# Kernel optimization log

Measured on AMD Instinct MI355X. Metric: run time of the kernel, lower is better.

Reference implementation:

```python
import jax, jax.numpy as jnp
import numpy as np

N, M = 50000, 2048          # nodes, observations
E, O = 512, 256             # in_features_embed, in_features_obs
EPS = 1e-6


def setup_inputs() -> dict:
    key = jax.random.key(0)
    k1, k2, k3, k4, k5 = jax.random.split(key, 5)
    scale_e = 1.0 / np.sqrt(E)
    scale_o = 1.0 / np.sqrt(O)
    return {
        "node_feature": jax.random.normal(k1, (N, E), dtype=jnp.float32),
        "obs_feature": jax.random.normal(k2, (M, O), dtype=jnp.float32),
        # nn.Linear weights, stored as [out, in] like torch
        "W_q": jax.random.normal(k3, (E, E), dtype=jnp.float32) * scale_e,
        "W_k": jax.random.normal(k4, (E, O), dtype=jnp.float32) * scale_o,
        "W_v": jax.random.normal(k5, (E, O), dtype=jnp.float32) * scale_o,
        "ln_gamma": jnp.ones((E,), dtype=jnp.float32),
        "ln_beta": jnp.zeros((E,), dtype=jnp.float32),
    }


def layer_norm(x, gamma, beta, eps=EPS):
    mu = jnp.mean(x, axis=-1, keepdims=True)
    var = jnp.mean(jnp.square(x - mu), axis=-1, keepdims=True)
    return (x - mu) * jax.lax.rsqrt(var + eps) * gamma + beta


def reference(node_feature, obs_feature, W_q, W_k, W_v, ln_gamma, ln_beta):
    # projections (torch Linear: x @ W.T)
    q = node_feature @ W_q.T            # [N, E]
    k = obs_feature @ W_k.T             # [M, E]
    v = obs_feature @ W_v.T             # [M, E]
    # un-normalized cross-attention (no softmax), original association
    attn = q @ k.T                      # [N, M]
    out = attn @ v                      # [N, E]
    return layer_norm(out + node_feature, ln_gamma, ln_beta)
```

## Files before the change

### kernel.cpp

```cpp
#include <hip/hip_runtime.h>
#include <hip/hip_bf16.h>

#define NROWS 50000
#define MOBS  2048
#define EDIM  512
#define ODIM  256

typedef short s16x8 __attribute__((ext_vector_type(8)));
typedef float f32x4 __attribute__((ext_vector_type(4)));

__device__ __forceinline__ unsigned short f32_to_bf16(float f) {
    unsigned int u = __float_as_uint(f);
    u += 0x7fffu + ((u >> 16) & 1u);
    return (unsigned short)(u >> 16);
}

template <int TA, int TB, int SPLIT, int FRAG>
__global__ __launch_bounds__(256) void sgemm4(const float* __restrict__ A,
                                              const float* __restrict__ B,
                                              void* __restrict__ Cv,
                                              int NN, int KK, int lda, int ldb) {
    __shared__ float SA[16][68];
    __shared__ float SB[16][68];
    const int t  = threadIdx.x;
    const int tx = t & 15, ty = t >> 4;
    const int i0 = blockIdx.y * 64, j0 = blockIdx.x * 64;
    int k_lo = 0, k_hi = KK;
    if (SPLIT > 1) { int ch = KK / SPLIT; k_lo = blockIdx.z * ch; k_hi = k_lo + ch; }

    float acc[4][4];
#pragma unroll
    for (int a = 0; a < 4; ++a)
#pragma unroll
        for (int b = 0; b < 4; ++b) acc[a][b] = 0.f;

    for (int k0 = k_lo; k0 < k_hi; k0 += 16) {
#pragma unroll
        for (int r = 0; r < 4; ++r) {
            int idx = t + 256 * r;
            int mm, kk2;
            if (TA) { mm = idx & 63; kk2 = idx >> 6; }
            else    { kk2 = idx & 15; mm = idx >> 4; }
            SA[kk2][mm] = TA ? A[(size_t)(k0 + kk2) * lda + i0 + mm]
                             : A[(size_t)(i0 + mm) * lda + k0 + kk2];
        }
#pragma unroll
        for (int r = 0; r < 4; ++r) {
            int idx = t + 256 * r;
            int jj, kk2;
            if (TB) { kk2 = idx & 15; jj = idx >> 4; }
            else    { jj = idx & 63; kk2 = idx >> 6; }
            SB[kk2][jj] = TB ? B[(size_t)(j0 + jj) * ldb + k0 + kk2]
                             : B[(size_t)(k0 + kk2) * ldb + j0 + jj];
        }
        __syncthreads();
#pragma unroll
        for (int kk2 = 0; kk2 < 16; ++kk2) {
            float4 a4 = *(const float4*)&SA[kk2][ty * 4];
            float4 b4 = *(const float4*)&SB[kk2][tx * 4];
            float av[4] = {a4.x, a4.y, a4.z, a4.w};
            float bv[4] = {b4.x, b4.y, b4.z, b4.w};
#pragma unroll
            for (int a = 0; a < 4; ++a)
#pragma unroll
                for (int b = 0; b < 4; ++b) acc[a][b] += av[a] * bv[b];
        }
        __syncthreads();
    }

    if (FRAG) {
        unsigned short* C = (unsigned short*)Cv;
#pragma unroll
        for (int a = 0; a < 4; ++a)
#pragma unroll
            for (int b = 0; b < 4; ++b) {
                int i = i0 + ty * 4 + a;
                int j = j0 + tx * 4 + b;
                float v = acc[a][b] + (i == j ? 1.f : 0.f);
                int f = j >> 4, lr = j & 15, kk = i >> 5, lk = (i >> 3) & 3;
                C[((size_t)((f * 16 + kk) * 64 + lk * 16 + lr)) * 8 + (i & 7)] =
                    f32_to_bf16(v);
            }
    } else if (SPLIT > 1) {
        float* C = (float*)Cv;
#pragma unroll
        for (int a = 0; a < 4; ++a)
#pragma unroll
            for (int b = 0; b < 4; ++b)
                atomicAdd(&C[(size_t)(i0 + ty * 4 + a) * NN + j0 + tx * 4 + b],
                          acc[a][b]);
    } else {
        float* C = (float*)Cv;
#pragma unroll
        for (int a = 0; a < 4; ++a) {
            float4 o = make_float4(acc[a][0], acc[a][1], acc[a][2], acc[a][3]);
            *(float4*)&C[(size_t)(i0 + ty * 4 + a) * NN + j0 + tx * 4] = o;
        }
    }
}

__global__ __launch_bounds__(256, 2) void gemm_mfma_ln(
    const float* __restrict__ node, const unsigned short* __restrict__ Uf,
    const float* __restrict__ gamma, const float* __restrict__ beta,
    float* __restrict__ out) {
    __shared__ unsigned short As[64 * 512];
    float* lds_s  = (float*)As;
    float* lds_q  = (float*)As + 256;
    float* lds_mu = (float*)As + 512;
    float* lds_rs = (float*)As + 576;

    const int t  = threadIdx.x;
    const int w  = t >> 6;
    const int l  = t & 63;
    const int lr = l & 15;
    const int lk = l >> 4;
    const int m0 = blockIdx.x * 64;

#pragma unroll 4
    for (int rb = 0; rb < 16; ++rb) {
        int row = rb * 4 + w;
        int gr = m0 + row;
        if (gr > NROWS - 1) gr = NROWS - 1;
        const float4* p = (const float4*)(node + (size_t)gr * EDIM + l * 8);
        float4 f0 = p[0], f1 = p[1];
        s16x8 av;
        av[0] = (short)f32_to_bf16(f0.x); av[1] = (short)f32_to_bf16(f0.y);
        av[2] = (short)f32_to_bf16(f0.z); av[3] = (short)f32_to_bf16(f0.w);
        av[4] = (short)f32_to_bf16(f1.x); av[5] = (short)f32_to_bf16(f1.y);
        av[6] = (short)f32_to_bf16(f1.z); av[7] = (short)f32_to_bf16(f1.w);
        int byte = row * 1024 + ((l * 16) ^ ((row & 7) << 4));
        *(s16x8*)((char*)As + byte) = av;
    }
    __syncthreads();

    f32x4 acc[4][8];
#pragma unroll
    for (int mi = 0; mi < 4; ++mi)
#pragma unroll
        for (int ni = 0; ni < 8; ++ni)
            acc[mi][ni] = (f32x4){0.f, 0.f, 0.f, 0.f};

    const unsigned short* bw = Uf + (size_t)w * 65536 + (size_t)l * 8;

    s16x8 bfr[2][8];
#pragma unroll
    for (int ni = 0; ni < 8; ++ni)
        bfr[0][ni] = *(const s16x8*)(bw + (size_t)ni * 8192);

#pragma unroll
    for (int kk = 0; kk < 16; ++kk) {
        const int cur = kk & 1, nxt = cur ^ 1;
        if (kk < 15) {
#pragma unroll
            for (int ni = 0; ni < 8; ++ni)
                bfr[nxt][ni] =
                    *(const s16x8*)(bw + (size_t)ni * 8192 + (kk + 1) * 512);
        }
        s16x8 afr[4];
#pragma unroll
        for (int mi = 0; mi < 4; ++mi) {
            int row = mi * 16 + lr;
            int byte = row * 1024 + ((kk * 64 + lk * 16) ^ ((row & 7) << 4));
            afr[mi] = *(const s16x8*)((const char*)As + byte);
        }
#pragma unroll
        for (int mi = 0; mi < 4; ++mi)
#pragma unroll
            for (int ni = 0; ni < 8; ++ni)
                acc[mi][ni] = __builtin_amdgcn_mfma_f32_16x16x32_bf16(
                    afr[mi], bfr[cur][ni], acc[mi][ni], 0, 0, 0);
    }

    __syncthreads();

#pragma unroll
    for (int mi = 0; mi < 4; ++mi) {
#pragma unroll
        for (int j = 0; j < 4; ++j) {
            float s = 0.f, q = 0.f;
#pragma unroll
            for (int ni = 0; ni < 8; ++ni) {
                float v = acc[mi][ni][j];
                s += v; q += v * v;
            }
#pragma unroll
            for (int off = 1; off < 16; off <<= 1) {
                s += __shfl_xor(s, off);
                q += __shfl_xor(q, off);
            }
            if (lr == 0) {
                int rl = mi * 16 + lk * 4 + j;
                lds_s[w * 64 + rl] = s;
                lds_q[w * 64 + rl] = q;
            }
        }
    }
    __syncthreads();
    if (t < 64) {
        float s = lds_s[t] + lds_s[64 + t] + lds_s[128 + t] + lds_s[192 + t];
        float q = lds_q[t] + lds_q[64 + t] + lds_q[128 + t] + lds_q[192 + t];
        float mu  = s * (1.f / (float)EDIM);
        float var = q * (1.f / (float)EDIM) - mu * mu;
        lds_mu[t] = mu;
        lds_rs[t] = rsqrtf(var + 1e-6f);
    }
    __syncthreads();

    const int n0 = w * 128;
    float gv[8], bv[8];
#pragma unroll
    for (int ni = 0; ni < 8; ++ni) {
        int c = n0 + ni * 16 + lr;
        gv[ni] = gamma[c];
        bv[ni] = beta[c];
    }

#pragma unroll
    for (int mi = 0; mi < 4; ++mi) {
#pragma unroll
        for (int j = 0; j < 4; ++j) {
            int rl = mi * 16 + lk * 4 + j;
            int gr = m0 + rl;
            if (gr < NROWS) {
                float mu = lds_mu[rl], rs = lds_rs[rl];
                float* op = out + (size_t)gr * EDIM + n0 + lr;
#pragma unroll
                for (int ni = 0; ni < 8; ++ni)
                    op[ni * 16] = (acc[mi][ni][j] - mu) * rs * gv[ni] + bv[ni];
            }
        }
    }
}

extern "C" void kernel_launch(void* const* d_in, const int* in_sizes, int n_in,
                              void* d_out, int out_size, void* d_ws, size_t ws_size,
                              hipStream_t stream) {
    const float* node  = (const float*)d_in[0];
    const float* obs   = (const float*)d_in[1];
    const float* Wq    = (const float*)d_in[2];
    const float* Wk    = (const float*)d_in[3];
    const float* Wv    = (const float*)d_in[4];
    const float* gamma = (const float*)d_in[5];
    const float* beta  = (const float*)d_in[6];
    float* out = (float*)d_out;

    float* ws = (float*)d_ws;
    float*          G  = ws;
    float*          P  = G  + ODIM * ODIM;
    float*          PG = P  + EDIM * ODIM;
    unsigned short* Uf = (unsigned short*)(PG + EDIM * ODIM);

    hipMemsetAsync((void*)G, 0,
                   (ODIM * ODIM + 2 * EDIM * ODIM) * sizeof(float), stream);

    sgemm4<1, 0, 16, 0><<<dim3(4, 4, 16), 256, 0, stream>>>(obs, obs, G, ODIM, MOBS, ODIM, ODIM);
    sgemm4<1, 0, 4, 0><<<dim3(4, 8, 4), 256, 0, stream>>>(Wq, Wk, P, ODIM, EDIM, EDIM, ODIM);
    sgemm4<0, 0, 2, 0><<<dim3(4, 8, 2), 256, 0, stream>>>(P, G, PG, ODIM, ODIM, ODIM, ODIM);
    sgemm4<0, 1, 1, 1><<<dim3(8, 8, 1), 256, 0, stream>>>(PG, Wv, Uf, EDIM, ODIM, ODIM, ODIM);
    gemm_mfma_ln<<<dim3((NROWS + 63) / 64), 256, 0, stream>>>(node, Uf, gamma, beta, out);
}
```

Before: 142.7 us.

## Merge Gram and projection GEMMs into one launch; use 8 waves in main GEMM

The two small setup GEMMs (obs^T obs and Wq^T Wk) are combined into a single kernel launch that dispatches on blockIdx.z, which removes one launch and lets both run concurrently. The main MFMA+LayerNorm kernel moves from 4 waves to 8 waves per 64-row block, and each wave now covers 64 output columns instead of 128. This halves the per-wave accumulators and B fragments, which should allow higher occupancy and better latency hiding on this memory-bound pass. The cost is more cross-wave reduction in the LayerNorm statistics and more redundant A-tile reads from LDS.

```diff
diff --git a/kernel.cpp b/kernel.cpp
--- a/kernel.cpp
+++ b/kernel.cpp
@@ -13,6 +13,70 @@
     unsigned int u = __float_as_uint(f);
     u += 0x7fffu + ((u >> 16) & 1u);
     return (unsigned short)(u >> 16);
+}
+
+__global__ __launch_bounds__(256) void gp_fused(const float* __restrict__ obs,
+                                                const float* __restrict__ Wq,
+                                                const float* __restrict__ Wk,
+                                                float* __restrict__ G,
+                                                float* __restrict__ P) {
+    __shared__ float SA[16][68];
+    __shared__ float SB[16][68];
+    const float *A, *B;
+    float* C;
+    int lda, ldb, k_lo, k_hi;
+    const int bz = blockIdx.z;
+    if (bz < 16) {
+        if (blockIdx.y >= 4) return;
+        A = obs; B = obs; C = G; lda = ODIM; ldb = ODIM;
+        k_lo = bz * (MOBS / 16); k_hi = k_lo + MOBS / 16;
+    } else {
+        A = Wq; B = Wk; C = P; lda = EDIM; ldb = ODIM;
+        k_lo = (bz - 16) * (EDIM / 4); k_hi = k_lo + EDIM / 4;
+    }
+    const int t  = threadIdx.x;
+    const int tx = t & 15, ty = t >> 4;
+    const int i0 = blockIdx.y * 64, j0 = blockIdx.x * 64;
+
+    float acc[4][4];
+#pragma unroll
+    for (int a = 0; a < 4; ++a)
+#pragma unroll
+        for (int b = 0; b < 4; ++b) acc[a][b] = 0.f;
+
+    for (int k0 = k_lo; k0 < k_hi; k0 += 16) {
+#pragma unroll
+        for (int r = 0; r < 4; ++r) {
+            int idx = t + 256 * r;
+            int mm = idx & 63, kk2 = idx >> 6;
+            SA[kk2][mm] = A[(size_t)(k0 + kk2) * lda + i0 + mm];
+        }
+#pragma unroll
+        for (int r = 0; r < 4; ++r) {
+            int idx = t + 256 * r;
+            int jj = idx & 63, kk2 = idx >> 6;
+            SB[kk2][jj] = B[(size_t)(k0 + kk2) * ldb + j0 + jj];
+        }
+        __syncthreads();
+#pragma unroll
+        for (int kk2 = 0; kk2 < 16; ++kk2) {
+            float4 a4 = *(const float4*)&SA[kk2][ty * 4];
+            float4 b4 = *(const float4*)&SB[kk2][tx * 4];
+            float av[4] = {a4.x, a4.y, a4.z, a4.w};
+            float bv[4] = {b4.x, b4.y, b4.z, b4.w};
+#pragma unroll
+            for (int a = 0; a < 4; ++a)
+#pragma unroll
+                for (int b = 0; b < 4; ++b) acc[a][b] += av[a] * bv[b];
+        }
+        __syncthreads();
+    }
+#pragma unroll
+    for (int a = 0; a < 4; ++a)
+#pragma unroll
+        for (int b = 0; b < 4; ++b)
+            atomicAdd(&C[(size_t)(i0 + ty * 4 + a) * ODIM + j0 + tx * 4 + b],
+                      acc[a][b]);
 }
 
 template <int TA, int TB, int SPLIT, int FRAG>
@@ -99,15 +163,15 @@
     }
 }
 
-__global__ __launch_bounds__(256, 2) void gemm_mfma_ln(
+__global__ __launch_bounds__(512, 4) void gemm_mfma_ln(
     const float* __restrict__ node, const unsigned short* __restrict__ Uf,
     const float* __restrict__ gamma, const float* __restrict__ beta,
     float* __restrict__ out) {
     __shared__ unsigned short As[64 * 512];
     float* lds_s  = (float*)As;
-    float* lds_q  = (float*)As + 256;
-    float* lds_mu = (float*)As + 512;
-    float* lds_rs = (float*)As + 576;
+    float* lds_q  = (float*)As + 512;
+    float* lds_mu = (float*)As + 1024;
+    float* lds_rs = (float*)As + 1088;
 
     const int t  = threadIdx.x;
     const int w  = t >> 6;
@@ -116,9 +180,9 @@
     const int lk = l >> 4;
     const int m0 = blockIdx.x * 64;
 
-#pragma unroll 4
-    for (int rb = 0; rb < 16; ++rb) {
-        int row = rb * 4 + w;
+#pragma unroll
+    for (int it = 0; it < 8; ++it) {
+        int row = it * 8 + w;
         int gr = m0 + row;
         if (gr > NROWS - 1) gr = NROWS - 1;
         const float4* p = (const float4*)(node + (size_t)gr * EDIM + l * 8);
@@ -133,18 +197,18 @@
     }
     __syncthreads();
 
-    f32x4 acc[4][8];
+    f32x4 acc[4][4];
 #pragma unroll
     for (int mi = 0; mi < 4; ++mi)
 #pragma unroll
-        for (int ni = 0; ni < 8; ++ni)
+        for (int ni = 0; ni < 4; ++ni)
             acc[mi][ni] = (f32x4){0.f, 0.f, 0.f, 0.f};
 
-    const unsigned short* bw = Uf + (size_t)w * 65536 + (size_t)l * 8;
-
-    s16x8 bfr[2][8];
-#pragma unroll
-    for (int ni = 0; ni < 8; ++ni)
+    const unsigned short* bw = Uf + (size_t)w * 32768 + (size_t)l * 8;
+
+    s16x8 bfr[2][4];
+#pragma unroll
+    for (int ni = 0; ni < 4; ++ni)
         bfr[0][ni] = *(const s16x8*)(bw + (size_t)ni * 8192);
 
 #pragma unroll
@@ -152,7 +216,7 @@
         const int cur = kk & 1, nxt = cur ^ 1;
         if (kk < 15) {
 #pragma unroll
-            for (int ni = 0; ni < 8; ++ni)
+            for (int ni = 0; ni < 4; ++ni)
                 bfr[nxt][ni] =
                     *(const s16x8*)(bw + (size_t)ni * 8192 + (kk + 1) * 512);
         }
@@ -166,7 +230,7 @@
 #pragma unroll
         for (int mi = 0; mi < 4; ++mi)
 #pragma unroll
-            for (int ni = 0; ni < 8; ++ni)
+            for (int ni = 0; ni < 4; ++ni)
                 acc[mi][ni] = __builtin_amdgcn_mfma_f32_16x16x32_bf16(
                     afr[mi], bfr[cur][ni], acc[mi][ni], 0, 0, 0);
     }
@@ -179,7 +243,7 @@
         for (int j = 0; j < 4; ++j) {
             float s = 0.f, q = 0.f;
 #pragma unroll
-            for (int ni = 0; ni < 8; ++ni) {
+            for (int ni = 0; ni < 4; ++ni) {
                 float v = acc[mi][ni][j];
                 s += v; q += v * v;
             }
@@ -197,8 +261,12 @@
     }
     __syncthreads();
     if (t < 64) {
-        float s = lds_s[t] + lds_s[64 + t] + lds_s[128 + t] + lds_s[192 + t];
-        float q = lds_q[t] + lds_q[64 + t] + lds_q[128 + t] + lds_q[192 + t];
+        float s = 0.f, q = 0.f;
+#pragma unroll
+        for (int ww = 0; ww < 8; ++ww) {
+            s += lds_s[ww * 64 + t];
+            q += lds_q[ww * 64 + t];
+        }
         float mu  = s * (1.f / (float)EDIM);
         float var = q * (1.f / (float)EDIM) - mu * mu;
         lds_mu[t] = mu;
@@ -206,10 +274,10 @@
     }
     __syncthreads();
 
-    const int n0 = w * 128;
-    float gv[8], bv[8];
-#pragma unroll
-    for (int ni = 0; ni < 8; ++ni) {
+    const int n0 = w * 64;
+    float gv[4], bv[4];
+#pragma unroll
+    for (int ni = 0; ni < 4; ++ni) {
         int c = n0 + ni * 16 + lr;
         gv[ni] = gamma[c];
         bv[ni] = beta[c];
@@ -225,7 +293,7 @@
                 float mu = lds_mu[rl], rs = lds_rs[rl];
                 float* op = out + (size_t)gr * EDIM + n0 + lr;
 #pragma unroll
-                for (int ni = 0; ni < 8; ++ni)
+                for (int ni = 0; ni < 4; ++ni)
                     op[ni * 16] = (acc[mi][ni][j] - mu) * rs * gv[ni] + bv[ni];
             }
         }
@@ -253,9 +321,8 @@
     hipMemsetAsync((void*)G, 0,
                    (ODIM * ODIM + 2 * EDIM * ODIM) * sizeof(float), stream);
 
-    sgemm4<1, 0, 16, 0><<<dim3(4, 4, 16), 256, 0, stream>>>(obs, obs, G, ODIM, MOBS, ODIM, ODIM);
-    sgemm4<1, 0, 4, 0><<<dim3(4, 8, 4), 256, 0, stream>>>(Wq, Wk, P, ODIM, EDIM, EDIM, ODIM);
+    gp_fused<<<dim3(4, 8, 20), 256, 0, stream>>>(obs, Wq, Wk, G, P);
     sgemm4<0, 0, 2, 0><<<dim3(4, 8, 2), 256, 0, stream>>>(P, G, PG, ODIM, ODIM, ODIM, ODIM);
     sgemm4<0, 1, 1, 1><<<dim3(8, 8, 1), 256, 0, stream>>>(PG, Wv, Uf, EDIM, ODIM, ODIM, ODIM);
-    gemm_mfma_ln<<<dim3((NROWS + 63) / 64), 256, 0, stream>>>(node, Uf, gamma, beta, out);
-}
+    gemm_mfma_ln<<<dim3((NROWS + 63) / 64), 512, 0, stream>>>(node, Uf, gamma, beta, out);
+}
```

Measured after the change: 129.6 us. -9.2%, faster.
